# Performance work log

Measured on AMD Instinct MI355X. Metric: run time of the kernel, lower is better.

The kernel has to match this reference:

```python
import jax, jax.numpy as jnp
import numpy as np

NEG_INF = -jnp.inf


def setup_inputs() -> dict:
    key = jax.random.key(0)
    k1, k2, k3 = jax.random.split(key, 3)
    B, S, D_IN, E = 16, 2048, 1024, 1024
    feats = jax.random.normal(k1, (B * S, D_IN), dtype=jnp.float32)
    masks = (jax.random.uniform(k2, (B * S, 1)) > 0.1).astype(jnp.float32)
    W = jax.random.normal(k3, (D_IN, E), dtype=jnp.float32) * 0.02
    b = jnp.zeros((E,), dtype=jnp.float32)
    return {"feats": feats, "masks": masks, "W": W, "b": b, "num_steps": S}


def reference(feats, masks, W, b, num_steps):
    B = feats.shape[0] // num_steps
    feats = feats.reshape(B, num_steps, feats.shape[-1])          # (B,S,D_in)
    x = jnp.einsum("bsd,de->bse", feats, W) + b                   # feats_proj

    masks_seq = (masks.reshape(B, num_steps, -1) != 0).any(-1)    # (B,S) bool
    masks_f = masks_seq.astype(x.dtype)

    # position ids: cumsum of mask, zeroed where mask == 0
    position_ids = jnp.where(masks_seq, jnp.cumsum(masks_f, axis=1), 0.0)

    # episodic attention mask: episode_start[j] = last k<=j with mask==0 (default 0)
    idx = jnp.arange(num_steps)                                   # (S,)
    start_cand = jnp.where(masks_seq, 0, idx[None, :])            # (B,S)
    ep_start = jax.lax.associative_scan(jnp.maximum, start_cand, axis=1)  # cummax
    allowed = (idx[None, None, :] >= ep_start[:, :, None]) & (
        idx[None, None, :] <= idx[None, :, None]
    )                                                             # (B,S,S)
    attn_mask = jnp.where(allowed, 0.0, NEG_INF).astype(x.dtype)
    return x, position_ids, attn_mask
```

## Files before the change

### kernel.cpp

```cpp
#include <hip/hip_runtime.h>


typedef unsigned int uint;
typedef unsigned short ushort;
typedef __attribute__((ext_vector_type(8))) short bf16x8;
typedef __attribute__((ext_vector_type(4))) float f32x4;
typedef __attribute__((ext_vector_type(8))) ushort u16x8;

__device__ __forceinline__ ushort f2bf_rtn(float x) {
    uint u = __float_as_uint(x);
    uint r = (u + 0x7FFFu + ((u >> 16) & 1u)) >> 16;
    return (ushort)r;
}

__device__ __forceinline__ int lidx2(int row, int chunk) {
    return row * 128 + ((chunk ^ (row & 7)) << 3);
}

#define LDS_BARRIER() do {                                        \
    __builtin_amdgcn_sched_barrier(0);                            \
    asm volatile("s_waitcnt lgkmcnt(0)" ::: "memory");            \
    __builtin_amdgcn_s_barrier();                                 \
    __builtin_amdgcn_sched_barrier(0);                            \
} while (0)

__global__ __launch_bounds__(256) void wsplit1_k(
    const float* __restrict__ W, ushort* __restrict__ Wh, int K, int N)
{
    __shared__ float tile[32][33];
    const int n0 = blockIdx.x * 32, k0 = blockIdx.y * 32;
    const int t = threadIdx.x;
    {
        const int nn = t & 31, kk = t >> 5;
        #pragma unroll
        for (int i = 0; i < 4; ++i)
            tile[kk + i * 8][nn] = W[(size_t)(k0 + kk + i * 8) * N + n0 + nn];
    }
    __syncthreads();
    {
        const int kk = t & 31, nn = t >> 5;
        #pragma unroll
        for (int i = 0; i < 4; ++i) {
            float x = tile[kk][nn + i * 8];
            Wh[(size_t)(n0 + nn + i * 8) * K + k0 + kk] = f2bf_rtn(x);
        }
    }
}

__global__ __launch_bounds__(256) void scan_k(
    const float* __restrict__ masks, float* __restrict__ pos_out,
    int* __restrict__ ep_out, int S)
{
    const int b = blockIdx.x, t = threadIdx.x;
    const float* mrow = masks + (size_t)b * S;

    float ls[8]; int lm[8]; bool on8[8];
    float csum = 0.0f; int cmax = 0;
    #pragma unroll
    for (int e = 0; e < 8; ++e) {
        const int j = t * 8 + e;
        const bool on = (mrow[j] != 0.0f);
        on8[e] = on;
        csum += on ? 1.0f : 0.0f;
        if (!on && j > cmax) cmax = j;
        ls[e] = csum;
        lm[e] = cmax;
    }
    __shared__ float ps[256];
    __shared__ int   pm[256];
    ps[t] = csum; pm[t] = cmax;
    __syncthreads();
    for (int off = 1; off < 256; off <<= 1) {
        float s = 0.0f; int m = 0;
        if (t >= off) { s = ps[t - off]; m = pm[t - off]; }
        __syncthreads();
        if (t >= off) { ps[t] += s; pm[t] = (m > pm[t]) ? m : pm[t]; }
        __syncthreads();
    }
    const float esum = (t == 0) ? 0.0f : ps[t - 1];
    const int   emax = (t == 0) ? 0    : pm[t - 1];
    #pragma unroll
    for (int e = 0; e < 8; ++e) {
        const int j = t * 8 + e;
        pos_out[(size_t)b * S + j] = on8[e] ? (esum + ls[e]) : 0.0f;
        const int ep = (lm[e] > emax) ? lm[e] : emax;
        ep_out[(size_t)b * S + j] = ep;
    }
}

__global__ __launch_bounds__(512, 1) void mfma_gemm18_k(
    const float* __restrict__ A, const ushort* __restrict__ Bh,
    const float* __restrict__ bias, float* __restrict__ C,
    const int* __restrict__ ep_ws, float* __restrict__ mask_out,
    int M, int N, int K, int S)
{
    __shared__ ushort Ls[2][256 * 128];

    const int tid  = threadIdx.x;
    const int lane = tid & 63, wv = tid >> 6;
    const int wr   = wv >> 2,  wc = wv & 3;

    const int lin  = blockIdx.x;
    const int wgid = (lin & 7) * 64 + (lin >> 3);
    const int bm = wgid >> 2, bn = wgid & 3;

    const int srow = tid >> 1;
    const int sh   = tid & 1;

    const float*  Ag  = A  + ((size_t)(bm * 256) + srow) * K;
    const ushort* Bhg = Bh + ((size_t)(bn * 256) + srow) * K;

    float4 a_st[8];
    u16x8  b_st[4];

    auto gload = [&](int kt) {
        const int kb = kt * 64 + sh * 32;
        const float* p = Ag + kb;
        #pragma unroll
        for (int i = 0; i < 8; ++i)
            a_st[i] = *(const float4*)(p + i * 4);
        const ushort* q = Bhg + kb;
        #pragma unroll
        for (int c = 0; c < 4; ++c)
            b_st[c] = *(const u16x8*)(q + c * 8);
    };

    auto lwrite = [&](int buf) {
        #pragma unroll
        for (int c = 0; c < 4; ++c) {
            u16x8 vh;
            float xs[8] = {a_st[2 * c].x,     a_st[2 * c].y,
                           a_st[2 * c].z,     a_st[2 * c].w,
                           a_st[2 * c + 1].x, a_st[2 * c + 1].y,
                           a_st[2 * c + 1].z, a_st[2 * c + 1].w};
            #pragma unroll
            for (int j = 0; j < 8; ++j)
                vh[j] = f2bf_rtn(xs[j]);
            *(u16x8*)&Ls[buf][lidx2(srow, sh * 4 + c)]     = vh;
            *(u16x8*)&Ls[buf][lidx2(srow, 8 + sh * 4 + c)] = b_st[c];
        }
    };

    f32x4 acc[8][4] = {};

    const int arow0 = wr * 128 + (lane & 15);
    const int brow0 = wc * 64  + (lane & 15);
    const int fq    = lane >> 4;

    const int mrow  = lin * 64 + (tid >> 3);
    const int irow  = mrow & (S - 1);
    const int ep    = ep_ws[mrow];
    const int l8    = tid & 7;
    f32x4* mbase    = (f32x4*)(mask_out + (size_t)mrow * S) + l8;
    const float NEG_BIG = -1.0e30f;

    gload(0);
    lwrite(0);
    __syncthreads();

    int cur = 0;
    const int NT = K / 64;
    for (int kt = 0; kt < NT; ++kt) {
        if (kt + 1 < NT) gload(kt + 1);

        #pragma unroll
        for (int u = 0; u < 4; ++u) {
            const int f  = l8 + 8 * (4 * kt + u);
            const int c0 = f * 4;
            f32x4 v;
            if (c0 >= ep && c0 + 3 <= irow) {
                v = (f32x4){0.0f, 0.0f, 0.0f, 0.0f};
            } else if (c0 + 3 < ep || c0 > irow) {
                v = (f32x4){NEG_BIG, NEG_BIG, NEG_BIG, NEG_BIG};
            } else {
                v[0] = (c0     >= ep && c0     <= irow) ? 0.0f : NEG_BIG;
                v[1] = (c0 + 1 >= ep && c0 + 1 <= irow) ? 0.0f : NEG_BIG;
                v[2] = (c0 + 2 >= ep && c0 + 2 <= irow) ? 0.0f : NEG_BIG;
                v[3] = (c0 + 3 >= ep && c0 + 3 <= irow) ? 0.0f : NEG_BIG;
            }
            __builtin_nontemporal_store(v, mbase + 8 * (4 * kt + u));
        }

        #pragma unroll
        for (int j2 = 0; j2 < 2; ++j2) {
            bf16x8 fb[4];
            #pragma unroll
            for (int ni = 0; ni < 4; ++ni)
                fb[ni] = *(const bf16x8*)&Ls[cur][lidx2(brow0 + ni * 16, 8 + j2 * 4 + fq)];
            #pragma unroll
            for (int h = 0; h < 2; ++h) {
                const int rbase = arow0 + h * 64;
                bf16x8 ah[4];
                #pragma unroll
                for (int mi = 0; mi < 4; ++mi)
                    ah[mi] = *(const bf16x8*)&Ls[cur][lidx2(rbase + mi * 16, j2 * 4 + fq)];
                #pragma unroll
                for (int mi = 0; mi < 4; ++mi)
                    #pragma unroll
                    for (int ni = 0; ni < 4; ++ni)
                        acc[h * 4 + mi][ni] = __builtin_amdgcn_mfma_f32_16x16x32_bf16(
                            ah[mi], fb[ni], acc[h * 4 + mi][ni], 0, 0, 0);
            }
        }

        if (kt + 1 < NT) {
            lwrite(cur ^ 1);
            LDS_BARRIER();
            cur ^= 1;
        }
    }

    const int crow = (lane >> 4) * 4;
    #pragma unroll
    for (int ni = 0; ni < 4; ++ni) {
        const int n = bn * 256 + wc * 64 + ni * 16 + (lane & 15);
        const float bv = bias[n];
        #pragma unroll
        for (int mi = 0; mi < 8; ++mi) {
            const int m0 = bm * 256 + wr * 128 + mi * 16 + crow;
            #pragma unroll
            for (int jj = 0; jj < 4; ++jj)
                __builtin_nontemporal_store(acc[mi][ni][jj] + bv,
                                            &C[(size_t)(m0 + jj) * N + n]);
        }
    }
}

#define BM 128
#define BN 128
#define BK 16

__global__ __launch_bounds__(256) void proj_gemm_k(
    const float* __restrict__ A, const float* __restrict__ B,
    const float* __restrict__ bias, float* __restrict__ C,
    int M, int N, int K)
{
    constexpr int LA = BM + 4;
    constexpr int LB = BN + 4;
    __shared__ __align__(16) float As[2][BK][LA];
    __shared__ __align__(16) float Bs[2][BK][LB];

    const int tid = threadIdx.x;
    const int bn  = blockIdx.x;
    const int bm  = blockIdx.y;
    const int ty  = tid >> 4;
    const int tx  = tid & 15;

    const float* Ag = A + (size_t)bm * BM * K;
    const float* Bg = B + (size_t)bn * BN;

    const int fa_r = tid >> 2;
    const int fa_c = (tid & 3) * 4;
    const int fb_k = tid >> 5;
    const int fb_c = (tid & 31) * 4;

    const int NT = K / BK;
    float acc[2][2][4][4] = {};
    float4 a0r, a1r, b0r, b1r;

    auto write_tile = [&](int buf) {
        As[buf][fa_c + 0][fa_r] = a0r.x;
        As[buf][fa_c + 1][fa_r] = a0r.y;
        As[buf][fa_c + 2][fa_r] = a0r.z;
        As[buf][fa_c + 3][fa_r] = a0r.w;
        As[buf][fa_c + 0][fa_r + 64] = a1r.x;
        As[buf][fa_c + 1][fa_r + 64] = a1r.y;
        As[buf][fa_c + 2][fa_r + 64] = a1r.z;
        As[buf][fa_c + 3][fa_r + 64] = a1r.w;
        *(float4*)&Bs[buf][fb_k][fb_c]     = b0r;
        *(float4*)&Bs[buf][fb_k + 8][fb_c] = b1r;
    };
    auto load_tile = [&](int kt) {
        const float* ap = Ag + kt * BK;
        a0r = *(const float4*)(ap + (size_t)fa_r * K + fa_c);
        a1r = *(const float4*)(ap + (size_t)(fa_r + 64) * K + fa_c);
        const float* bp = Bg + (size_t)kt * BK * N;
        b0r = *(const float4*)(bp + (size_t)fb_k * N + fb_c);
        b1r = *(const float4*)(bp + (size_t)(fb_k + 8) * N + fb_c);
    };

    load_tile(0);
    write_tile(0);
    __syncthreads();

    int cur = 0;
    for (int kt = 0; kt < NT; ++kt) {
        if (kt + 1 < NT) load_tile(kt + 1);
        #pragma unroll
        for (int k = 0; k < BK; ++k) {
            float4 x0 = *(const float4*)&As[cur][k][ty * 4];
            float4 x1 = *(const float4*)&As[cur][k][64 + ty * 4];
            float4 y0 = *(const float4*)&Bs[cur][k][tx * 4];
            float4 y1 = *(const float4*)&Bs[cur][k][64 + tx * 4];
            float avv[2][4] = {{x0.x, x0.y, x0.z, x0.w}, {x1.x, x1.y, x1.z, x1.w}};
            float bvv[2][4] = {{y0.x, y0.y, y0.z, y0.w}, {y1.x, y1.y, y1.z, y1.w}};
            #pragma unroll
            for (int mi = 0; mi < 2; ++mi)
                #pragma unroll
                for (int i = 0; i < 4; ++i)
                    #pragma unroll
                    for (int ni = 0; ni < 2; ++ni)
                        #pragma unroll
                        for (int jj = 0; jj < 4; ++jj)
                            acc[mi][ni][i][jj] = fmaf(avv[mi][i], bvv[ni][jj], acc[mi][ni][i][jj]);
        }
        if (kt + 1 < NT) {
            write_tile(cur ^ 1);
            __syncthreads();
            cur ^= 1;
        }
    }

    #pragma unroll
    for (int ni = 0; ni < 2; ++ni) {
        const int n = bn * BN + ni * 64 + tx * 4;
        float4 bv = *(const float4*)&bias[n];
        #pragma unroll
        for (int mi = 0; mi < 2; ++mi) {
            #pragma unroll
            for (int i = 0; i < 4; ++i) {
                const int m = bm * BM + mi * 64 + ty * 4 + i;
                float4 o;
                o.x = acc[mi][ni][i][0] + bv.x;
                o.y = acc[mi][ni][i][1] + bv.y;
                o.z = acc[mi][ni][i][2] + bv.z;
                o.w = acc[mi][ni][i][3] + bv.w;
                *(float4*)(C + (size_t)m * N + n) = o;
            }
        }
    }
}

__global__ __launch_bounds__(256) void episodic_mask_k(
    const float* __restrict__ masks, float* __restrict__ pos_out,
    float* __restrict__ mask_out, int S)
{
    const int i = blockIdx.x;
    const int b = blockIdx.y;
    const int t = threadIdx.x;
    const float* mrow = masks + (size_t)b * S;

    float sum = 0.0f;
    int   mx  = 0;
    for (int j = t; j <= i; j += 256) {
        const bool on = (mrow[j] != 0.0f);
        sum += on ? 1.0f : 0.0f;
        if (!on && j > mx) mx = j;
    }
    #pragma unroll
    for (int off = 32; off > 0; off >>= 1) {
        sum += __shfl_down(sum, off, 64);
        int o = __shfl_down(mx, off, 64);
        mx = (o > mx) ? o : mx;
    }
    __shared__ float wsum[4];
    __shared__ int   wmax[4];
    __shared__ int   s_ep;
    const int wid = t >> 6, lane = t & 63;
    if (lane == 0) { wsum[wid] = sum; wmax[wid] = mx; }
    __syncthreads();
    if (t == 0) {
        float ts = wsum[0] + wsum[1] + wsum[2] + wsum[3];
        int tm = wmax[0];
        tm = (wmax[1] > tm) ? wmax[1] : tm;
        tm = (wmax[2] > tm) ? wmax[2] : tm;
        tm = (wmax[3] > tm) ? wmax[3] : tm;
        s_ep = tm;
        pos_out[(size_t)b * S + i] = (mrow[i] != 0.0f) ? ts : 0.0f;
    }
    __syncthreads();
    const int ep = s_ep;
    const float NEG_BIG = -1.0e30f;
    float4* orow = (float4*)(mask_out + ((size_t)b * S + i) * S);
    const int nf = S >> 2;
    for (int f = t; f < nf; f += 256) {
        const int j0 = f * 4;
        float4 v;
        v.x = (j0     >= ep && j0     <= i) ? 0.0f : NEG_BIG;
        v.y = (j0 + 1 >= ep && j0 + 1 <= i) ? 0.0f : NEG_BIG;
        v.z = (j0 + 2 >= ep && j0 + 2 <= i) ? 0.0f : NEG_BIG;
        v.w = (j0 + 3 >= ep && j0 + 3 <= i) ? 0.0f : NEG_BIG;
        orow[f] = v;
    }
}

extern "C" void kernel_launch(void* const* d_in, const int* in_sizes, int n_in,
                              void* d_out, int out_size, void* d_ws, size_t ws_size,
                              hipStream_t stream)
{
    const float* feats = (const float*)d_in[0];
    const float* masks = (const float*)d_in[1];
    const float* W     = (const float*)d_in[2];
    const float* bias  = (const float*)d_in[3];

    const int M = in_sizes[1];
    const int K = in_sizes[0] / M;
    const int N = in_sizes[3];
    const int S = out_size / M - N - 1;
    const int B = M / S;

    float* x_out    = (float*)d_out;
    float* pos_out  = x_out + (size_t)M * N;
    float* mask_out = pos_out + M;

    const size_t w_w   = (size_t)K * N * sizeof(ushort);
    const size_t w_all = w_w + (size_t)M * sizeof(int);

    if (ws_size >= w_all && S == 2048 && (M % 64) == 0 && (K % 64) == 0) {
        ushort* Wh = (ushort*)d_ws;
        int*    ep = (int*)(Wh + (size_t)K * N);
        wsplit1_k<<<dim3(N / 32, K / 32), 256, 0, stream>>>(W, Wh, K, N);
        scan_k<<<B, 256, 0, stream>>>(masks, pos_out, ep, S);
        const int nblk = (M / 256) * (N / 256);
        mfma_gemm18_k<<<nblk, 512, 0, stream>>>(
            feats, Wh, bias, x_out, ep, mask_out, M, N, K, S);
    } else {
        proj_gemm_k<<<dim3(N / BN, M / BM), 256, 0, stream>>>(feats, W, bias, x_out, M, N, K);
        episodic_mask_k<<<dim3(S, B), 256, 0, stream>>>(masks, pos_out, mask_out, S);
    }
}
```

Before: 179.6 us.

## Shrink fused GEMM tile to 128x128x32 with 256 threads and remap blocks

The fused projection GEMM and mask writer drops from 256x256 tiles with K-step 64 and 512 threads to 128x128 tiles with K-step 32 and 256 threads. This quadruples the block count to 2048, and each block now writes 16 mask rows instead of 64. The block-to-tile mapping changes so each XCD handles a contiguous band of row tiles across all column tiles. The smaller LDS footprint and fewer accumulators allow more blocks per CU and better load balance, at the cost of more reloads of A and W per tile and more barriers per unit of work.

```diff
diff --git a/kernel.cpp b/kernel.cpp
--- a/kernel.cpp
+++ b/kernel.cpp
@@ -13,8 +13,8 @@
     return (ushort)r;
 }
 
-__device__ __forceinline__ int lidx2(int row, int chunk) {
-    return row * 128 + ((chunk ^ (row & 7)) << 3);
+__device__ __forceinline__ int lidx(int row, int chunk) {
+    return row * 64 + ((chunk ^ (row & 7)) << 3);
 }
 
 #define LDS_BARRIER() do {                                        \
@@ -88,46 +88,46 @@
     }
 }
 
-__global__ __launch_bounds__(512, 1) void mfma_gemm18_k(
+__global__ __launch_bounds__(256, 1) void mfma_gemm19_k(
     const float* __restrict__ A, const ushort* __restrict__ Bh,
     const float* __restrict__ bias, float* __restrict__ C,
     const int* __restrict__ ep_ws, float* __restrict__ mask_out,
     int M, int N, int K, int S)
 {
-    __shared__ ushort Ls[2][256 * 128];
+    __shared__ ushort Ls[2][128 * 64];
 
     const int tid  = threadIdx.x;
     const int lane = tid & 63, wv = tid >> 6;
-    const int wr   = wv >> 2,  wc = wv & 3;
-
-    const int lin  = blockIdx.x;
-    const int wgid = (lin & 7) * 64 + (lin >> 3);
-    const int bm = wgid >> 2, bn = wgid & 3;
+    const int wr   = wv >> 1,  wc = wv & 1;
+
+    const int lin = blockIdx.x;
+    const int xcd = lin & 7, sblk = lin >> 3;
+    const int bm  = xcd * 32 + (sblk >> 3);
+    const int bn  = sblk & 7;
 
     const int srow = tid >> 1;
     const int sh   = tid & 1;
 
-    const float*  Ag  = A  + ((size_t)(bm * 256) + srow) * K;
-    const ushort* Bhg = Bh + ((size_t)(bn * 256) + srow) * K;
-
-    float4 a_st[8];
-    u16x8  b_st[4];
+    const float*  Ag  = A  + ((size_t)(bm * 128) + srow) * K;
+    const ushort* Bhg = Bh + ((size_t)(bn * 128) + srow) * K;
+
+    float4 a_st[4];
+    u16x8  b_st[2];
 
     auto gload = [&](int kt) {
-        const int kb = kt * 64 + sh * 32;
+        const int kb = kt * 32 + sh * 16;
         const float* p = Ag + kb;
         #pragma unroll
-        for (int i = 0; i < 8; ++i)
+        for (int i = 0; i < 4; ++i)
             a_st[i] = *(const float4*)(p + i * 4);
         const ushort* q = Bhg + kb;
-        #pragma unroll
-        for (int c = 0; c < 4; ++c)
-            b_st[c] = *(const u16x8*)(q + c * 8);
+        b_st[0] = *(const u16x8*)q;
+        b_st[1] = *(const u16x8*)(q + 8);
     };
 
     auto lwrite = [&](int buf) {
         #pragma unroll
-        for (int c = 0; c < 4; ++c) {
+        for (int c = 0; c < 2; ++c) {
             u16x8 vh;
             float xs[8] = {a_st[2 * c].x,     a_st[2 * c].y,
                            a_st[2 * c].z,     a_st[2 * c].w,
@@ -136,22 +136,22 @@
             #pragma unroll
             for (int j = 0; j < 8; ++j)
                 vh[j] = f2bf_rtn(xs[j]);
-            *(u16x8*)&Ls[buf][lidx2(srow, sh * 4 + c)]     = vh;
-            *(u16x8*)&Ls[buf][lidx2(srow, 8 + sh * 4 + c)] = b_st[c];
+            *(u16x8*)&Ls[buf][lidx(srow, sh * 2 + c)]     = vh;
+            *(u16x8*)&Ls[buf][lidx(srow, 4 + sh * 2 + c)] = b_st[c];
         }
     };
 
-    f32x4 acc[8][4] = {};
-
-    const int arow0 = wr * 128 + (lane & 15);
-    const int brow0 = wc * 64  + (lane & 15);
+    f32x4 acc[4][4] = {};
+
+    const int arow0 = wr * 64 + (lane & 15);
+    const int brow0 = wc * 64 + (lane & 15);
     const int fq    = lane >> 4;
 
-    const int mrow  = lin * 64 + (tid >> 3);
+    const int mrow  = lin * 16 + (tid >> 4);
     const int irow  = mrow & (S - 1);
     const int ep    = ep_ws[mrow];
-    const int l8    = tid & 7;
-    f32x4* mbase    = (f32x4*)(mask_out + (size_t)mrow * S) + l8;
+    const int l16   = tid & 15;
+    f32x4* mbase    = (f32x4*)(mask_out + (size_t)mrow * S) + l16;
     const float NEG_BIG = -1.0e30f;
 
     gload(0);
@@ -159,13 +159,12 @@
     __syncthreads();
 
     int cur = 0;
-    const int NT = K / 64;
+    const int NT = K / 32;
     for (int kt = 0; kt < NT; ++kt) {
         if (kt + 1 < NT) gload(kt + 1);
 
-        #pragma unroll
-        for (int u = 0; u < 4; ++u) {
-            const int f  = l8 + 8 * (4 * kt + u);
+        {
+            const int f  = l16 + 16 * kt;
             const int c0 = f * 4;
             f32x4 v;
             if (c0 >= ep && c0 + 3 <= irow) {
@@ -178,30 +177,22 @@
                 v[2] = (c0 + 2 >= ep && c0 + 2 <= irow) ? 0.0f : NEG_BIG;
                 v[3] = (c0 + 3 >= ep && c0 + 3 <= irow) ? 0.0f : NEG_BIG;
             }
-            __builtin_nontemporal_store(v, mbase + 8 * (4 * kt + u));
-        }
-
-        #pragma unroll
-        for (int j2 = 0; j2 < 2; ++j2) {
-            bf16x8 fb[4];
+            __builtin_nontemporal_store(v, mbase + 16 * kt);
+        }
+
+        bf16x8 fb[4], ah[4];
+        #pragma unroll
+        for (int ni = 0; ni < 4; ++ni)
+            fb[ni] = *(const bf16x8*)&Ls[cur][lidx(brow0 + ni * 16, 4 + fq)];
+        #pragma unroll
+        for (int mi = 0; mi < 4; ++mi)
+            ah[mi] = *(const bf16x8*)&Ls[cur][lidx(arow0 + mi * 16, fq)];
+        #pragma unroll
+        for (int mi = 0; mi < 4; ++mi)
             #pragma unroll
             for (int ni = 0; ni < 4; ++ni)
-                fb[ni] = *(const bf16x8*)&Ls[cur][lidx2(brow0 + ni * 16, 8 + j2 * 4 + fq)];
-            #pragma unroll
-            for (int h = 0; h < 2; ++h) {
-                const int rbase = arow0 + h * 64;
-                bf16x8 ah[4];
-                #pragma unroll
-                for (int mi = 0; mi < 4; ++mi)
-                    ah[mi] = *(const bf16x8*)&Ls[cur][lidx2(rbase + mi * 16, j2 * 4 + fq)];
-                #pragma unroll
-                for (int mi = 0; mi < 4; ++mi)
-                    #pragma unroll
-                    for (int ni = 0; ni < 4; ++ni)
-                        acc[h * 4 + mi][ni] = __builtin_amdgcn_mfma_f32_16x16x32_bf16(
-                            ah[mi], fb[ni], acc[h * 4 + mi][ni], 0, 0, 0);
-            }
-        }
+                acc[mi][ni] = __builtin_amdgcn_mfma_f32_16x16x32_bf16(
+                    ah[mi], fb[ni], acc[mi][ni], 0, 0, 0);
 
         if (kt + 1 < NT) {
             lwrite(cur ^ 1);
@@ -213,11 +204,11 @@
     const int crow = (lane >> 4) * 4;
     #pragma unroll
     for (int ni = 0; ni < 4; ++ni) {
-        const int n = bn * 256 + wc * 64 + ni * 16 + (lane & 15);
+        const int n = bn * 128 + wc * 64 + ni * 16 + (lane & 15);
         const float bv = bias[n];
         #pragma unroll
-        for (int mi = 0; mi < 8; ++mi) {
-            const int m0 = bm * 256 + wr * 128 + mi * 16 + crow;
+        for (int mi = 0; mi < 4; ++mi) {
+            const int m0 = bm * 128 + wr * 64 + mi * 16 + crow;
             #pragma unroll
             for (int jj = 0; jj < 4; ++jj)
                 __builtin_nontemporal_store(acc[mi][ni][jj] + bv,
@@ -406,13 +397,13 @@
     const size_t w_w   = (size_t)K * N * sizeof(ushort);
     const size_t w_all = w_w + (size_t)M * sizeof(int);
 
-    if (ws_size >= w_all && S == 2048 && (M % 64) == 0 && (K % 64) == 0) {
+    if (ws_size >= w_all && S == 2048 && (M % 16) == 0 && (K % 32) == 0) {
         ushort* Wh = (ushort*)d_ws;
         int*    ep = (int*)(Wh + (size_t)K * N);
         wsplit1_k<<<dim3(N / 32, K / 32), 256, 0, stream>>>(W, Wh, K, N);
         scan_k<<<B, 256, 0, stream>>>(masks, pos_out, ep, S);
-        const int nblk = (M / 256) * (N / 256);
-        mfma_gemm18_k<<<nblk, 512, 0, stream>>>(
+        const int nblk = (M / 128) * (N / 128);
+        mfma_gemm19_k<<<nblk, 256, 0, stream>>>(
             feats, Wh, bias, x_out, ep, mask_out, M, N, K, S);
     } else {
         proj_gemm_k<<<dim3(N / BN, M / BM), 256, 0, stream>>>(feats, W, bias, x_out, M, N, K);
```

After: 160.2 us. 1.12x faster.
